# Performance work log

Hardware: AMD Instinct MI355X
Metric: run time of the kernel (lower is better)

## Reference

```python
import jax, jax.numpy as jnp
import numpy as np

N, D, K, M = 1024, 128, 256, 4
H, NB = 256, 2  # QINCoStep defaults: hidden_dim=256, num_res_blocks=2


def setup_inputs() -> dict:
    key = jax.random.key(0)
    ks = jax.random.split(key, 6)
    z = jax.random.normal(ks[0], (N, D), jnp.float32)
    base_cb = jax.random.normal(ks[1], (M, K, D), jnp.float32) * 0.1
    cp_w = jax.random.normal(ks[2], (M, D, 2 * D), jnp.float32) * (1.0 / np.sqrt(2 * D)).astype(np.float32)
    cp_b = jnp.zeros((M, D), jnp.float32)
    w1 = jax.random.normal(ks[3], (M, NB, H, D), jnp.float32) * (1.0 / np.sqrt(D)).astype(np.float32)
    b1 = jnp.zeros((M, NB, H), jnp.float32)
    w2 = jax.random.normal(ks[4], (M, NB, D, H), jnp.float32) * (1.0 / np.sqrt(H)).astype(np.float32)
    b2 = jnp.zeros((M, NB, D), jnp.float32)
    return dict(z=z, base_cb=base_cb, cp_w=cp_w, cp_b=cp_b, w1=w1, b1=b1, w2=w2, b2=b2)


def _encode_step(z, x_hat, cb, cpw, cpb, w1, b1, w2, b2):
    # concat_proj(Linear(2D,D)) on cat([x_hat, cbar]) decomposed into two GEMMs
    Wx, Wc = cpw[:, :D], cpw[:, D:]          # (D,D), (D,D)
    A = x_hat @ Wx.T                          # (N,D)
    B = cb @ Wc.T                             # (K,D)
    C = A[:, None, :] + B[None, :, :] + cpb   # (N,K,D) data-dependent codebook
    for i in range(NB):                       # residual MLP blocks
        h = jax.nn.relu(jnp.einsum('nkd,hd->nkh', C, w1[i]) + b1[i])
        C = C + jnp.einsum('nkh,dh->nkd', h, w2[i]) + b2[i]
    r = z - x_hat                             # (N,D) residual before step
    dists = jnp.sum((r[:, None, :] - C) ** 2, axis=-1)   # (N,K)
    codes = jnp.argmin(dists, axis=-1)        # (N,)
    c_sel = jnp.take_along_axis(C, codes[:, None, None], axis=1)[:, 0]  # (N,D)
    return codes, x_hat + c_sel, r, c_sel


def reference(z, base_cb, cp_w, cp_b, w1, b1, w2, b2):
    x_hat = jnp.zeros_like(z)
    codes_all, residuals, centroids = [], [], []
    for m in range(M):
        codes, x_hat, r, c_sel = _encode_step(
            z, x_hat, base_cb[m], cp_w[m], cp_b[m], w1[m], b1[m], w2[m], b2[m])
        codes_all.append(codes)
        residuals.append(r)
        centroids.append(c_sel)
    codes_all = jnp.stack(codes_all, axis=-1)          # (N,M)
    z_q = x_hat
    z_q_st = z + jax.lax.stop_gradient(z_q - z)        # straight-through
    return z_q_st, codes_all, jnp.stack(residuals), jnp.stack(centroids)
```

## Files before the change

### kernel.cpp

```cpp
#include <hip/hip_runtime.h>

#define N_ 1024
#define D_ 128
#define K_ 256
#define M_ 4
#define H_ 256
#define NB_ 2
#define KT_ 64
#define NTILE_ 4
#define EPS_ 0.12f
#define CHPAD 136
#define HPAD  264

typedef _Float16 half8 __attribute__((ext_vector_type(8)));
typedef __attribute__((ext_vector_type(8))) short short8;
typedef __attribute__((ext_vector_type(4))) float f32x4;
typedef __attribute__((ext_vector_type(16))) float f32x16;

__device__ inline float s2f(unsigned short s) {
    return (float)__builtin_bit_cast(_Float16, s);
}
__device__ inline unsigned short f2h(float x) {
    return __builtin_bit_cast(unsigned short, (_Float16)x);
}
__device__ inline void split2h(float x, unsigned short& hi, unsigned short& lo) {
    _Float16 h = (_Float16)x;
    _Float16 l = (_Float16)(x - (float)h);
    hi = __builtin_bit_cast(unsigned short, h);
    lo = __builtin_bit_cast(unsigned short, l);
}
__device__ inline f32x16 zero16() {
    f32x16 v;
    #pragma unroll
    for (int i = 0; i < 16; ++i) v[i] = 0.0f;
    return v;
}
__device__ inline void lds_barrier() {
    asm volatile("s_waitcnt lgkmcnt(0)" ::: "memory");
    __builtin_amdgcn_sched_barrier(0);
    __builtin_amdgcn_s_barrier();
    __builtin_amdgcn_sched_barrier(0);
}

__global__ void precompute_Bb(const float* __restrict__ base_cb,
                              const float* __restrict__ cp_w,
                              float* __restrict__ Bb) {
    const int mk = blockIdx.x;
    const int m  = mk >> 8;
    const int d  = threadIdx.x;
    const float* cb = base_cb + (size_t)mk * D_;
    const float* wc = cp_w + ((size_t)(m * D_ + d)) * (2 * D_) + D_;
    double a0 = 0, a1 = 0, a2 = 0, a3 = 0;
    #pragma unroll
    for (int dp = 0; dp < D_; dp += 4) {
        a0 += (double)(cb[dp + 0] * wc[dp + 0]);
        a1 += (double)(cb[dp + 1] * wc[dp + 1]);
        a2 += (double)(cb[dp + 2] * wc[dp + 2]);
        a3 += (double)(cb[dp + 3] * wc[dp + 3]);
    }
    Bb[(size_t)mk * D_ + d] = (float)((a0 + a1) + (a2 + a3));
}

__global__ void convert_w(const float* __restrict__ w1,
                          const float* __restrict__ w2,
                          unsigned short* __restrict__ w1pk,
                          unsigned short* __restrict__ w2pk) {
    const int i = blockIdx.x * blockDim.x + threadIdx.x;
    {
        const int e    = i & 7;
        const int sel  = (i >> 3) & 1;
        const int j32  = (i >> 4) & 31;
        const int kt   = (i >> 9) & 7;
        const int jblk = (i >> 12) & 7;
        const int bi   = i >> 15;
        const int j = jblk * 32 + j32;
        const int d = kt * 16 + sel * 8 + e;
        w1pk[i] = f2h(w1[((size_t)(bi * H_ + j)) * D_ + d]);
    }
    {
        const int e    = i & 7;
        const int sel  = (i >> 3) & 1;
        const int d32  = (i >> 4) & 31;
        const int s    = (i >> 9) & 15;
        const int dblk = (i >> 13) & 3;
        const int bi   = i >> 15;
        const int d = dblk * 32 + d32;
        const int hc = s * 16 + sel * 8 + e;
        w2pk[i] = f2h(w2[((size_t)(bi * D_ + d)) * H_ + hc]);
    }
}

__launch_bounds__(256, 2)
__global__ void mega_kernel(const float* __restrict__ z,
                            const float* __restrict__ cp_w,
                            const float* __restrict__ cp_b,
                            const float* __restrict__ w1,
                            const float* __restrict__ b1,
                            const float* __restrict__ w2,
                            const float* __restrict__ b2,
                            const float* __restrict__ Bb,
                            const unsigned short* __restrict__ w1pk,
                            const unsigned short* __restrict__ w2pk,
                            float* __restrict__ out0,
                            float* __restrict__ out1,
                            float* __restrict__ out2,
                            float* __restrict__ out3) {
    __shared__ alignas(16) unsigned short sChi[KT_][CHPAD];
    __shared__ alignas(16) unsigned short sClo[KT_][CHPAD];
    __shared__ alignas(16) unsigned short sHh[KT_][HPAD];
    __shared__ float sA[D_], sxhat[D_], sr[D_], scb[D_];
    __shared__ float sdist[K_];
    __shared__ float sE[D_], scsel[D_];
    __shared__ float shrow[H_];
    __shared__ double sdd[2];
    __shared__ float smin, sbest;
    __shared__ int   sbidx, supd;

    const int n    = blockIdx.x;
    const int t    = threadIdx.x;
    const int wid  = t >> 6;
    const int lane = t & 63;
    const int l31  = lane & 31;
    const int koff = (lane >> 5) * 8;
    const int loff = (l31 * 2 + (lane >> 5)) * 8;

    if (t < D_) { sxhat[t] = 0.0f; sA[t] = 0.0f; }
    __syncthreads();

    for (int m = 0; m < M_; ++m) {
        if (t < D_) {
            scb[t] = cp_b[m * D_ + t];
            const float rv = z[(size_t)n * D_ + t] - sxhat[t];
            sr[t] = rv;
            out2[((size_t)m * N_ + n) * D_ + t] = rv;
        }
        lds_barrier();

        for (int tile = 0; tile < NTILE_; ++tile) {
            const int k0 = tile * KT_;

            {
                const int row = t >> 2;
                const int cb0 = (t & 3) * 32;
                const f32x4* bb4 = (const f32x4*)(Bb + ((size_t)(m * K_ + k0 + row)) * D_ + cb0);
                #pragma unroll
                for (int g = 0; g < 4; ++g) {
                    const f32x4 v0 = bb4[g * 2];
                    const f32x4 v1 = bb4[g * 2 + 1];
                    short8 hs, ls;
                    #pragma unroll
                    for (int x = 0; x < 8; ++x) {
                        const int d = cb0 + g * 8 + x;
                        const float bv = (x < 4) ? v0[x] : v1[x - 4];
                        unsigned short ch, cl;
                        split2h((sA[d] + bv) + scb[d], ch, cl);
                        hs[x] = (short)ch;
                        ls[x] = (short)cl;
                    }
                    *(short8*)&sChi[row][cb0 + g * 8] = hs;
                    *(short8*)&sClo[row][cb0 + g * 8] = ls;
                }
            }
            lds_barrier();

            for (int i = 0; i < NB_; ++i) {
                const int bi = m * NB_ + i;

                half8 g2w[16];
                {
                    const int j0 = wid * 32 + l31;
                    const unsigned short* pA = w1pk + ((size_t)((bi * 8 + wid) * 8)) * 512 + loff;
                    const unsigned short* pB = w1pk + ((size_t)((bi * 8 + wid + 4) * 8)) * 512 + loff;
                    half8 wA[8], wB[8];
                    #pragma unroll
                    for (int kt = 0; kt < 8; ++kt) {
                        wA[kt] = *(const half8*)(pA + kt * 512);
                        wB[kt] = *(const half8*)(pB + kt * 512);
                    }
                    f32x16 aA0 = zero16(), aA1 = zero16();
                    f32x16 aB0 = zero16(), aB1 = zero16();
                    #pragma unroll
                    for (int kt = 0; kt < 8; ++kt) {
                        half8 ah0 = *(const half8*)&sChi[l31][kt * 16 + koff];
                        half8 al0 = *(const half8*)&sClo[l31][kt * 16 + koff];
                        half8 ah1 = *(const half8*)&sChi[32 + l31][kt * 16 + koff];
                        half8 al1 = *(const half8*)&sClo[32 + l31][kt * 16 + koff];
                        aA0 = __builtin_amdgcn_mfma_f32_32x32x16_f16(ah0, wA[kt], aA0, 0, 0, 0);
                        aB0 = __builtin_amdgcn_mfma_f32_32x32x16_f16(ah0, wB[kt], aB0, 0, 0, 0);
                        aA1 = __builtin_amdgcn_mfma_f32_32x32x16_f16(ah1, wA[kt], aA1, 0, 0, 0);
                        aB1 = __builtin_amdgcn_mfma_f32_32x32x16_f16(ah1, wB[kt], aB1, 0, 0, 0);
                        aA0 = __builtin_amdgcn_mfma_f32_32x32x16_f16(al0, wA[kt], aA0, 0, 0, 0);
                        aB0 = __builtin_amdgcn_mfma_f32_32x32x16_f16(al0, wB[kt], aB0, 0, 0, 0);
                        aA1 = __builtin_amdgcn_mfma_f32_32x32x16_f16(al1, wA[kt], aA1, 0, 0, 0);
                        aB1 = __builtin_amdgcn_mfma_f32_32x32x16_f16(al1, wB[kt], aB1, 0, 0, 0);
                    }
                    {
                        const unsigned short* pd =
                            w2pk + ((size_t)((bi * 4 + wid) * 16)) * 512 + loff;
                        #pragma unroll
                        for (int s = 0; s < 16; ++s)
                            g2w[s] = *(const half8*)(pd + s * 512);
                    }
                    const float b1A = b1[(size_t)bi * H_ + j0];
                    const float b1B = b1[(size_t)bi * H_ + j0 + 128];
                    #pragma unroll
                    for (int reg = 0; reg < 16; ++reg) {
                        const int krow = (reg & 3) + 8 * (reg >> 2) + 4 * (lane >> 5);
                        sHh[krow][j0]            = f2h(fmaxf(aA0[reg] + b1A, 0.0f));
                        sHh[32 + krow][j0]       = f2h(fmaxf(aA1[reg] + b1A, 0.0f));
                        sHh[krow][j0 + 128]      = f2h(fmaxf(aB0[reg] + b1B, 0.0f));
                        sHh[32 + krow][j0 + 128] = f2h(fmaxf(aB1[reg] + b1B, 0.0f));
                    }
                }
                lds_barrier();

                {
                    const int d = wid * 32 + l31;
                    f32x16 c0a = zero16(), c0b = zero16();
                    f32x16 c1a = zero16(), c1b = zero16();
                    #pragma unroll
                    for (int s = 0; s < 16; s += 2) {
                        half8 h0e = *(const half8*)&sHh[l31][s * 16 + koff];
                        half8 h1e = *(const half8*)&sHh[32 + l31][s * 16 + koff];
                        half8 h0o = *(const half8*)&sHh[l31][(s + 1) * 16 + koff];
                        half8 h1o = *(const half8*)&sHh[32 + l31][(s + 1) * 16 + koff];
                        c0a = __builtin_amdgcn_mfma_f32_32x32x16_f16(h0e, g2w[s], c0a, 0, 0, 0);
                        c1a = __builtin_amdgcn_mfma_f32_32x32x16_f16(h1e, g2w[s], c1a, 0, 0, 0);
                        c0b = __builtin_amdgcn_mfma_f32_32x32x16_f16(h0o, g2w[s + 1], c0b, 0, 0, 0);
                        c1b = __builtin_amdgcn_mfma_f32_32x32x16_f16(h1o, g2w[s + 1], c1b, 0, 0, 0);
                    }
                    const float b2v = b2[(size_t)bi * D_ + d];
                    #pragma unroll
                    for (int reg = 0; reg < 16; ++reg) {
                        const int krow = (reg & 3) + 8 * (reg >> 2) + 4 * (lane >> 5);
                        {
                            const float cvo = s2f(sChi[krow][d]) + s2f(sClo[krow][d]);
                            const float cv  = (cvo + (c0a[reg] + c0b[reg])) + b2v;
                            unsigned short ch, cl;
                            split2h(cv, ch, cl);
                            sChi[krow][d] = ch;
                            sClo[krow][d] = cl;
                        }
                        {
                            const int r2 = 32 + krow;
                            const float cvo = s2f(sChi[r2][d]) + s2f(sClo[r2][d]);
                            const float cv  = (cvo + (c1a[reg] + c1b[reg])) + b2v;
                            unsigned short ch, cl;
                            split2h(cv, ch, cl);
                            sChi[r2][d] = ch;
                            sClo[r2][d] = cl;
                        }
                    }
                }
                lds_barrier();
            }

            {
                const int row = t >> 2, seg = t & 3;
                float qa = 0.f;
                #pragma unroll
                for (int dd = 0; dd < 32; ++dd) {
                    const int d = seg * 32 + dd;
                    const float cv = s2f(sChi[row][d]) + s2f(sClo[row][d]);
                    const float e = sr[d] - cv;
                    qa = fmaf(e, e, qa);
                }
                qa += __shfl_xor(qa, 1);
                qa += __shfl_xor(qa, 2);
                if (seg == 0) sdist[k0 + row] = qa;
            }
            lds_barrier();
        }

        if (t < 64) {
            float bv = fminf(fminf(sdist[t], sdist[t + 64]),
                             fminf(sdist[t + 128], sdist[t + 192]));
            #pragma unroll
            for (int s = 1; s < 64; s <<= 1) bv = fminf(bv, __shfl_xor(bv, s));
            if (t == 0) { smin = bv; sbest = 1e30f; sbidx = 0; }
        }
        __syncthreads();
        const float thr = smin + EPS_;

        for (int k = 0; k < K_; ++k) {
            if (sdist[k] > thr) continue;
            if (t < D_)
                sE[t] = (sA[t] + Bb[((size_t)(m * K_ + k)) * D_ + t]) + scb[t];
            __syncthreads();
            for (int i = 0; i < NB_; ++i) {
                const int bi = m * NB_ + i;
                {
                    const f32x4* wp = (const f32x4*)(w1 + ((size_t)bi * H_ + t) * D_);
                    double h0 = 0, h1 = 0, h2 = 0, h3 = 0;
                    #pragma unroll 8
                    for (int u = 0; u < 32; ++u) {
                        f32x4 wv = wp[u];
                        h0 += (double)(sE[u * 4 + 0] * wv[0]);
                        h1 += (double)(sE[u * 4 + 1] * wv[1]);
                        h2 += (double)(sE[u * 4 + 2] * wv[2]);
                        h3 += (double)(sE[u * 4 + 3] * wv[3]);
                    }
                    const float hv = (float)((h0 + h1) + (h2 + h3)) + b1[(size_t)bi * H_ + t];
                    shrow[t] = fmaxf(hv, 0.0f);
                }
                __syncthreads();
                if (t < D_) {
                    const f32x4* wp = (const f32x4*)(w2 + ((size_t)bi * D_ + t) * H_);
                    double s0 = 0, s1 = 0, s2 = 0, s3 = 0;
                    #pragma unroll 8
                    for (int u = 0; u < 64; ++u) {
                        f32x4 wv = wp[u];
                        s0 += (double)(shrow[u * 4 + 0] * wv[0]);
                        s1 += (double)(shrow[u * 4 + 1] * wv[1]);
                        s2 += (double)(shrow[u * 4 + 2] * wv[2]);
                        s3 += (double)(shrow[u * 4 + 3] * wv[3]);
                    }
                    sE[t] = (sE[t] + (float)((s0 + s1) + (s2 + s3))) + b2[(size_t)bi * D_ + t];
                }
                __syncthreads();
            }
            {
                double dp = 0.0;
                if (t < D_) {
                    const float e = sr[t] - sE[t];
                    const float e2 = e * e;
                    dp = (double)e2;
                    #pragma unroll
                    for (int s = 1; s < 64; s <<= 1) dp += __shfl_xor(dp, s);
                    if ((t & 63) == 0) sdd[t >> 6] = dp;
                }
            }
            __syncthreads();
            if (t == 0) {
                const float df = (float)(sdd[0] + sdd[1]);
                if (df < sbest) { sbest = df; sbidx = k; supd = 1; }
                else supd = 0;
            }
            __syncthreads();
            if (supd && t < D_) scsel[t] = sE[t];
            __syncthreads();
        }

        if (t == 0) out1[(size_t)n * M_ + m] = (float)sbidx;

        if (t < D_) {
            const float cs = scsel[t];
            out3[((size_t)m * N_ + n) * D_ + t] = cs;
            const float xnew = sxhat[t] + cs;
            sxhat[t] = xnew;
            if (m == M_ - 1) {
                const float zv = z[(size_t)n * D_ + t];
                out0[(size_t)n * D_ + t] = zv + (xnew - zv);
            }
        }
        __syncthreads();

        if (m < M_ - 1 && t < D_) {
            const f32x4* wp = (const f32x4*)(cp_w + ((size_t)((m + 1) * D_ + t)) * (2 * D_));
            double a0 = 0, a1 = 0, a2 = 0, a3 = 0;
            #pragma unroll 8
            for (int u = 0; u < 32; ++u) {
                f32x4 wv = wp[u];
                a0 += (double)(sxhat[u * 4 + 0] * wv[0]);
                a1 += (double)(sxhat[u * 4 + 1] * wv[1]);
                a2 += (double)(sxhat[u * 4 + 2] * wv[2]);
                a3 += (double)(sxhat[u * 4 + 3] * wv[3]);
            }
            sA[t] = (float)((a0 + a1) + (a2 + a3));
        }
        __syncthreads();
    }
}

extern "C" void kernel_launch(void* const* d_in, const int* in_sizes, int n_in,
                              void* d_out, int out_size, void* d_ws, size_t ws_size,
                              hipStream_t stream) {
    const float* z       = (const float*)d_in[0];
    const float* base_cb = (const float*)d_in[1];
    const float* cp_w    = (const float*)d_in[2];
    const float* cp_b    = (const float*)d_in[3];
    const float* w1      = (const float*)d_in[4];
    const float* b1      = (const float*)d_in[5];
    const float* w2      = (const float*)d_in[6];
    const float* b2      = (const float*)d_in[7];

    float* out  = (float*)d_out;
    float* out0 = out;
    float* out1 = out0 + (size_t)N_ * D_;
    float* out2 = out1 + (size_t)N_ * M_;
    float* out3 = out2 + (size_t)M_ * N_ * D_;

    char* ws = (char*)d_ws;
    float*          Bb   = (float*)(ws + 0);
    unsigned short* w1pk = (unsigned short*)(ws + 524288);
    unsigned short* w2pk = (unsigned short*)(ws + 1048576);

    hipLaunchKernelGGL(precompute_Bb, dim3(M_ * K_), dim3(D_), 0, stream,
                       base_cb, cp_w, Bb);
    hipLaunchKernelGGL(convert_w, dim3(1024), dim3(256), 0, stream,
                       w1, w2, w1pk, w2pk);
    hipLaunchKernelGGL(mega_kernel, dim3(N_), dim3(256), 0, stream,
                       z, cp_w, cp_b, w1, b1, w2, b2, Bb,
                       w1pk, w2pk,
                       out0, out1, out2, out3);
}
```

Before: 949.5 us.

## Keep codebook tile in MFMA accumulator registers and store fp32 for distance

Precomputes a second copy of Bb in the MFMA accumulator lane layout, so each thread builds its slice of the codebook tile straight in registers. That slice then seeds the second GEMM's accumulator, which replaces the old read-modify-write of the hi/lo fp16 split in LDS for the residual add. The last residual block writes fp32 into a reused shared buffer, which the distance loop reads as vec4 instead of recombining hi/lo halves. This cuts LDS traffic and conversion work, at the cost of more register pressure from holding cr0/cr1 across the MLP and an extra workspace buffer.

```diff
diff --git a/kernel.cpp b/kernel.cpp
--- a/kernel.cpp
+++ b/kernel.cpp
@@ -10,6 +10,7 @@
 #define NTILE_ 4
 #define EPS_ 0.12f
 #define CHPAD 136
+#define CFS 140
 #define HPAD  264
 
 typedef _Float16 half8 __attribute__((ext_vector_type(8)));
@@ -44,9 +45,11 @@
 
 __global__ void precompute_Bb(const float* __restrict__ base_cb,
                               const float* __restrict__ cp_w,
-                              float* __restrict__ Bb) {
+                              float* __restrict__ Bb,
+                              float* __restrict__ Bbpk) {
     const int mk = blockIdx.x;
     const int m  = mk >> 8;
+    const int k  = mk & 255;
     const int d  = threadIdx.x;
     const float* cb = base_cb + (size_t)mk * D_;
     const float* wc = cp_w + ((size_t)(m * D_ + d)) * (2 * D_) + D_;
@@ -58,7 +61,17 @@
         a2 += (double)(cb[dp + 2] * wc[dp + 2]);
         a3 += (double)(cb[dp + 3] * wc[dp + 3]);
     }
-    Bb[(size_t)mk * D_ + d] = (float)((a0 + a1) + (a2 + a3));
+    const float v = (float)((a0 + a1) + (a2 + a3));
+    Bb[(size_t)mk * D_ + d] = v;
+
+    const int tile = k >> 6, rr = k & 63;
+    const int cg = rr >> 5, rr2 = rr & 31;
+    const int q = rr2 >> 3, hi = (rr2 >> 2) & 1, j = rr2 & 3;
+    const int run = (cg << 2) | q;
+    const int lane = (hi << 5) | (d & 31);
+    const int wid = d >> 5;
+    const size_t idx = ((((size_t)m * 4 + tile) * 4 + wid) * 8 + run) * 256 + lane * 4 + j;
+    Bbpk[idx] = v;
 }
 
 __global__ void convert_w(const float* __restrict__ w1,
@@ -99,30 +112,36 @@
                             const float* __restrict__ w2,
                             const float* __restrict__ b2,
                             const float* __restrict__ Bb,
+                            const float* __restrict__ Bbpk,
                             const unsigned short* __restrict__ w1pk,
                             const unsigned short* __restrict__ w2pk,
                             float* __restrict__ out0,
                             float* __restrict__ out1,
                             float* __restrict__ out2,
                             float* __restrict__ out3) {
-    __shared__ alignas(16) unsigned short sChi[KT_][CHPAD];
-    __shared__ alignas(16) unsigned short sClo[KT_][CHPAD];
+    __shared__ alignas(16) char sCbuf[35840];
     __shared__ alignas(16) unsigned short sHh[KT_][HPAD];
-    __shared__ float sA[D_], sxhat[D_], sr[D_], scb[D_];
-    __shared__ float sdist[K_];
+    __shared__ alignas(16) float sA[D_], sxhat[D_], sr[D_], scb[D_];
+    __shared__ alignas(16) float sdist[K_];
     __shared__ float sE[D_], scsel[D_];
     __shared__ float shrow[H_];
     __shared__ double sdd[2];
     __shared__ float smin, sbest;
     __shared__ int   sbidx, supd;
 
+    #define CHI(r, c) (((unsigned short*)sCbuf)[(r) * CHPAD + (c)])
+    #define CLO(r, c) (((unsigned short*)sCbuf)[8704 + (r) * CHPAD + (c)])
+    #define CF(r, c)  (((float*)sCbuf)[(r) * CFS + (c)])
+
     const int n    = blockIdx.x;
     const int t    = threadIdx.x;
     const int wid  = t >> 6;
     const int lane = t & 63;
     const int l31  = lane & 31;
-    const int koff = (lane >> 5) * 8;
-    const int loff = (l31 * 2 + (lane >> 5)) * 8;
+    const int hi   = lane >> 5;
+    const int koff = hi * 8;
+    const int loff = (l31 * 2 + hi) * 8;
+    const int dcol = wid * 32 + l31;
 
     if (t < D_) { sxhat[t] = 0.0f; sA[t] = 0.0f; }
     __syncthreads();
@@ -135,30 +154,34 @@
             out2[((size_t)m * N_ + n) * D_ + t] = rv;
         }
         lds_barrier();
+        const float aD  = sA[dcol];
+        const float cbD = scb[dcol];
 
         for (int tile = 0; tile < NTILE_; ++tile) {
             const int k0 = tile * KT_;
 
+            f32x16 cr0, cr1;
             {
-                const int row = t >> 2;
-                const int cb0 = (t & 3) * 32;
-                const f32x4* bb4 = (const f32x4*)(Bb + ((size_t)(m * K_ + k0 + row)) * D_ + cb0);
+                const float* bbp = Bbpk +
+                    ((((size_t)m * 4 + tile) * 4 + wid) * 8) * 256 + lane * 4;
                 #pragma unroll
-                for (int g = 0; g < 4; ++g) {
-                    const f32x4 v0 = bb4[g * 2];
-                    const f32x4 v1 = bb4[g * 2 + 1];
-                    short8 hs, ls;
-                    #pragma unroll
-                    for (int x = 0; x < 8; ++x) {
-                        const int d = cb0 + g * 8 + x;
-                        const float bv = (x < 4) ? v0[x] : v1[x - 4];
-                        unsigned short ch, cl;
-                        split2h((sA[d] + bv) + scb[d], ch, cl);
-                        hs[x] = (short)ch;
-                        ls[x] = (short)cl;
-                    }
-                    *(short8*)&sChi[row][cb0 + g * 8] = hs;
-                    *(short8*)&sClo[row][cb0 + g * 8] = ls;
+                for (int run = 0; run < 4; ++run) {
+                    const f32x4 b0 = *(const f32x4*)(bbp + run * 256);
+                    const f32x4 b1 = *(const f32x4*)(bbp + (run + 4) * 256);
+                    #pragma unroll
+                    for (int j = 0; j < 4; ++j) {
+                        cr0[run * 4 + j] = (aD + b0[j]) + cbD;
+                        cr1[run * 4 + j] = (aD + b1[j]) + cbD;
+                    }
+                }
+                #pragma unroll
+                for (int reg = 0; reg < 16; ++reg) {
+                    const int krow = (reg & 3) + 8 * (reg >> 2) + 4 * hi;
+                    unsigned short ch, cl;
+                    split2h(cr0[reg], ch, cl);
+                    CHI(krow, dcol) = ch; CLO(krow, dcol) = cl;
+                    split2h(cr1[reg], ch, cl);
+                    CHI(32 + krow, dcol) = ch; CLO(32 + krow, dcol) = cl;
                 }
             }
             lds_barrier();
@@ -181,10 +204,10 @@
                     f32x16 aB0 = zero16(), aB1 = zero16();
                     #pragma unroll
                     for (int kt = 0; kt < 8; ++kt) {
-                        half8 ah0 = *(const half8*)&sChi[l31][kt * 16 + koff];
-                        half8 al0 = *(const half8*)&sClo[l31][kt * 16 + koff];
-                        half8 ah1 = *(const half8*)&sChi[32 + l31][kt * 16 + koff];
-                        half8 al1 = *(const half8*)&sClo[32 + l31][kt * 16 + koff];
+                        half8 ah0 = *(const half8*)&CHI(l31, kt * 16 + koff);
+                        half8 al0 = *(const half8*)&CLO(l31, kt * 16 + koff);
+                        half8 ah1 = *(const half8*)&CHI(32 + l31, kt * 16 + koff);
+                        half8 al1 = *(const half8*)&CLO(32 + l31, kt * 16 + koff);
                         aA0 = __builtin_amdgcn_mfma_f32_32x32x16_f16(ah0, wA[kt], aA0, 0, 0, 0);
                         aB0 = __builtin_amdgcn_mfma_f32_32x32x16_f16(ah0, wB[kt], aB0, 0, 0, 0);
                         aA1 = __builtin_amdgcn_mfma_f32_32x32x16_f16(ah1, wA[kt], aA1, 0, 0, 0);
@@ -205,7 +228,7 @@
                     const float b1B = b1[(size_t)bi * H_ + j0 + 128];
                     #pragma unroll
                     for (int reg = 0; reg < 16; ++reg) {
-                        const int krow = (reg & 3) + 8 * (reg >> 2) + 4 * (lane >> 5);
+                        const int krow = (reg & 3) + 8 * (reg >> 2) + 4 * hi;
                         sHh[krow][j0]            = f2h(fmaxf(aA0[reg] + b1A, 0.0f));
                         sHh[32 + krow][j0]       = f2h(fmaxf(aA1[reg] + b1A, 0.0f));
                         sHh[krow][j0 + 128]      = f2h(fmaxf(aB0[reg] + b1B, 0.0f));
@@ -215,9 +238,8 @@
                 lds_barrier();
 
                 {
-                    const int d = wid * 32 + l31;
-                    f32x16 c0a = zero16(), c0b = zero16();
-                    f32x16 c1a = zero16(), c1b = zero16();
+                    f32x16 c0a = cr0, c0b = zero16();
+                    f32x16 c1a = cr1, c1b = zero16();
                     #pragma unroll
                     for (int s = 0; s < 16; s += 2) {
                         half8 h0e = *(const half8*)&sHh[l31][s * 16 + koff];
@@ -229,41 +251,46 @@
                         c0b = __builtin_amdgcn_mfma_f32_32x32x16_f16(h0o, g2w[s + 1], c0b, 0, 0, 0);
                         c1b = __builtin_amdgcn_mfma_f32_32x32x16_f16(h1o, g2w[s + 1], c1b, 0, 0, 0);
                     }
-                    const float b2v = b2[(size_t)bi * D_ + d];
+                    const float b2v = b2[(size_t)bi * D_ + dcol];
                     #pragma unroll
                     for (int reg = 0; reg < 16; ++reg) {
-                        const int krow = (reg & 3) + 8 * (reg >> 2) + 4 * (lane >> 5);
-                        {
-                            const float cvo = s2f(sChi[krow][d]) + s2f(sClo[krow][d]);
-                            const float cv  = (cvo + (c0a[reg] + c0b[reg])) + b2v;
-                            unsigned short ch, cl;
-                            split2h(cv, ch, cl);
-                            sChi[krow][d] = ch;
-                            sClo[krow][d] = cl;
-                        }
-                        {
-                            const int r2 = 32 + krow;
-                            const float cvo = s2f(sChi[r2][d]) + s2f(sClo[r2][d]);
-                            const float cv  = (cvo + (c1a[reg] + c1b[reg])) + b2v;
-                            unsigned short ch, cl;
-                            split2h(cv, ch, cl);
-                            sChi[r2][d] = ch;
-                            sClo[r2][d] = cl;
-                        }
+                        cr0[reg] = (c0a[reg] + c0b[reg]) + b2v;
+                        cr1[reg] = (c1a[reg] + c1b[reg]) + b2v;
+                    }
+                }
+                if (i < NB_ - 1) {
+                    #pragma unroll
+                    for (int reg = 0; reg < 16; ++reg) {
+                        const int krow = (reg & 3) + 8 * (reg >> 2) + 4 * hi;
+                        unsigned short ch, cl;
+                        split2h(cr0[reg], ch, cl);
+                        CHI(krow, dcol) = ch; CLO(krow, dcol) = cl;
+                        split2h(cr1[reg], ch, cl);
+                        CHI(32 + krow, dcol) = ch; CLO(32 + krow, dcol) = cl;
+                    }
+                } else {
+                    #pragma unroll
+                    for (int reg = 0; reg < 16; ++reg) {
+                        const int krow = (reg & 3) + 8 * (reg >> 2) + 4 * hi;
+                        CF(krow, dcol)      = cr0[reg];
+                        CF(32 + krow, dcol) = cr1[reg];
                     }
                 }
                 lds_barrier();
             }
 
             {
-                const int row = t >> 2, seg = t & 3;
+                const int row = t >> 2, seg = t & 3, db = seg * 32;
                 float qa = 0.f;
                 #pragma unroll
-                for (int dd = 0; dd < 32; ++dd) {
-                    const int d = seg * 32 + dd;
-                    const float cv = s2f(sChi[row][d]) + s2f(sClo[row][d]);
-                    const float e = sr[d] - cv;
-                    qa = fmaf(e, e, qa);
+                for (int g = 0; g < 8; ++g) {
+                    const f32x4 cv = *(const f32x4*)&CF(row, db + g * 4);
+                    const f32x4 rv = *(const f32x4*)&sr[db + g * 4];
+                    #pragma unroll
+                    for (int x = 0; x < 4; ++x) {
+                        const float e = rv[x] - cv[x];
+                        qa = fmaf(e, e, qa);
+                    }
                 }
                 qa += __shfl_xor(qa, 1);
                 qa += __shfl_xor(qa, 2);
@@ -370,6 +397,9 @@
         }
         __syncthreads();
     }
+    #undef CHI
+    #undef CLO
+    #undef CF
 }
 
 extern "C" void kernel_launch(void* const* d_in, const int* in_sizes, int n_in,
@@ -394,13 +424,14 @@
     float*          Bb   = (float*)(ws + 0);
     unsigned short* w1pk = (unsigned short*)(ws + 524288);
     unsigned short* w2pk = (unsigned short*)(ws + 1048576);
+    float*          Bbpk = (float*)(ws + 1572864);
 
     hipLaunchKernelGGL(precompute_Bb, dim3(M_ * K_), dim3(D_), 0, stream,
-                       base_cb, cp_w, Bb);
+                       base_cb, cp_w, Bb, Bbpk);
     hipLaunchKernelGGL(convert_w, dim3(1024), dim3(256), 0, stream,
                        w1, w2, w1pk, w2pk);
     hipLaunchKernelGGL(mega_kernel, dim3(N_), dim3(256), 0, stream,
-                       z, cp_w, cp_b, w1, b1, w2, b2, Bb,
+                       z, cp_w, cp_b, w1, b1, w2, b2, Bb, Bbpk,
                        w1pk, w2pk,
                        out0, out1, out2, out3);
 }
```

Measured after the change: 1.071 ms. 1.13x slower.
